# Kernel optimization log

Hardware: AMD Instinct MI355X
Metric: run time of the kernel (lower is better)

Reference implementation:

```python
import jax, jax.numpy as jnp
import numpy as np

N, M, D, DE, H, G = 2048, 16, 512, 128, 8, 50
DH, DEH, NF = D // H, DE // H, 4  # head dims; 2**2 frames for 2D frame averaging
OPS = jnp.array([[-1., -1.], [-1., 1.], [1., -1.], [1., 1.]], dtype=jnp.float32)

def ln(x, eps=1e-5):
    m = x.mean(-1, keepdims=True)
    v = x.var(-1, keepdims=True)
    return (x - m) * jax.lax.rsqrt(v + eps)

def mlp2(x, w1, b1, w2, b2):
    # timm-style Mlp with norm_layer=LayerNorm: fc1 -> GELU -> LN -> fc2 (dropout=0)
    h = jax.nn.gelu(x @ w1 + b1, approximate=False)
    return ln(h) @ w2 + b2

def setup_inputs():
    key = jax.random.key(0)
    ks = iter(jax.random.split(key, 32))
    def w(shape):
        return jax.random.normal(next(ks), shape, jnp.float32) / float(np.sqrt(shape[0]))
    return dict(
        gene_exp=jax.random.uniform(next(ks), (N, G), jnp.float32),
        token_embs=jax.random.normal(next(ks), (N, D), jnp.float32),
        coords=jax.random.uniform(next(ks), (N, 2), jnp.float32) * 100.0,
        neighbor_indices=jax.random.randint(next(ks), (N, M), 0, N),
        w_qkv=w((D, 3 * D)), b_qkv=jnp.zeros((3 * D,), jnp.float32),
        wa1=w((2 * DH + DEH + G, D)), ba1=jnp.zeros((D,), jnp.float32),
        wa2=w((D, 1)), ba2=jnp.zeros((1,), jnp.float32),
        we1=w((3, DE)), be1=jnp.zeros((DE,), jnp.float32),
        we2=w((DE, DE)), be2=jnp.zeros((DE,), jnp.float32),
        wo1=w((D + DE, D)), bo1=jnp.zeros((D,), jnp.float32),
        wo2=w((D, D)), bo2=jnp.zeros((D,), jnp.float32),
        wm1=w((D, 4 * D)), bm1=jnp.zeros((4 * D,), jnp.float32),
        wm2=w((4 * D, D)), bm2=jnp.zeros((D,), jnp.float32),
        wg1=w((D, D)), bg1=jnp.zeros((D,), jnp.float32),
        wg2=w((D, G)), bg2=jnp.zeros((G,), jnp.float32),
    )

def reference(gene_exp, token_embs, coords, neighbor_indices, w_qkv, b_qkv, wa1, ba1, wa2, ba2, we1, be1, we2, be2, wo1, bo1, wo2, bo2, wm1, bm1, wm2, bm2, wg1, bg1, wg2, bg2):
    qkv = ln(token_embs) @ w_qkv + b_qkv
    q, k, v = jnp.split(qkv, 3, axis=-1)
    q, k, v = (t.reshape(N, H, DH) for t in (q, k, v))
    # --- frame averaging over neighbor point clouds (dim=2 -> 4 sign frames) ---
    radial = coords[neighbor_indices] - coords[:, None, :]            # [N,M,2]
    rnorm = jnp.linalg.norm(radial, axis=-1, keepdims=True)           # [N,M,1]
    Xc = radial - radial.mean(axis=1, keepdims=True)
    C = jnp.einsum('nmi,nmj->nij', Xc, Xc)                            # [N,2,2]
    _, V = jnp.linalg.eigh(jax.lax.stop_gradient(C))                  # eigh on detached cov (as in torch code)
    proj = jnp.einsum('nmj,nji->nmi', Xc, V)                          # [N,M,2]
    frame = OPS[None, :, None, :] * proj[:, None, :, :]               # [N,4,M,2]
    rn = jnp.broadcast_to(rnorm[:, None], (N, NF, M, 1))
    edge = mlp2(jnp.concatenate([frame, rn], axis=-1), we1, be1, we2, be2).mean(axis=1)  # [N,M,DE]
    # --- per-edge MLP attention ---
    gd = gene_exp[neighbor_indices] - gene_exp[:, None, :]            # [N,M,G]
    msg = jnp.concatenate([
        jnp.broadcast_to(q[:, None], (N, M, H, DH)),
        k[neighbor_indices],
        edge.reshape(N, M, H, DEH),
        jnp.broadcast_to(gd[:, :, None, :], (N, M, H, G)),
    ], axis=-1)                                                       # [N,M,H,2*DH+DEH+G]
    logits = mlp2(msg, wa1, ba1, wa2, ba2)[..., 0]                    # [N,M,H]
    attn = jax.nn.softmax(logits.transpose(0, 2, 1), axis=-1)         # [N,H,M]
    # --- context aggregation ---
    sc = jnp.einsum('nhm,nmhd->nhd', attn, v[neighbor_indices]).reshape(N, D)
    ec = jnp.einsum('nhm,nmhd->nhd', attn, edge.reshape(N, M, H, DEH)).reshape(N, DE)
    ctx = mlp2(jnp.concatenate([sc, ec], axis=-1), wo1, bo1, wo2, bo2)
    tok = token_embs + ctx
    tok = tok + mlp2(tok, wm1, bm1, wm2, bm2)
    # gene updater: Linear -> GELU -> LN -> Linear
    gene_out = mlp2(tok, wg1, bg1, wg2, bg2)
    return gene_out, tok
```

## Files before the change

### kernel.cpp

```cpp
#include <hip/hip_runtime.h>
#include <math.h>

#define NN 2048
#define MM 16
#define DD 512
#define DE 128
#define HH 8
#define GG 50
#define DH 64
#define DEH 16

typedef __attribute__((ext_vector_type(8))) short bf8_t;
typedef __attribute__((ext_vector_type(4))) float f4_t;
typedef __attribute__((ext_vector_type(2))) float f2_t;
typedef unsigned short us;

__device__ __forceinline__ void gload16(const us* g, us* l) {
    __builtin_amdgcn_global_load_lds(
        (const __attribute__((address_space(1))) unsigned int*)g,
        (__attribute__((address_space(3))) unsigned int*)l, 16, 0, 0);
}

__device__ __forceinline__ float gelu_f(float x) {
    float u = 1.5957691216f * fmaf(0.044715f * x, x * x, x);
    u = fminf(fmaxf(u, -30.f), 30.f);
    float e = __expf(u);
    float t = fmaf(-2.f, __builtin_amdgcn_rcpf(e + 1.f), 1.f);
    float hx = 0.5f * x;
    return fmaf(hx, t, hx);
}

__device__ __forceinline__ f2_t gelu2(f2_t x) {
    f2_t u = ((x * 0.044715f) * (x * x) + x) * 1.5957691216f;
    f2_t e1;
    e1.x = __expf(u.x) + 1.f;
    e1.y = __expf(u.y) + 1.f;
    f2_t r;
    r.x = __builtin_amdgcn_rcpf(e1.x);
    r.y = __builtin_amdgcn_rcpf(e1.y);
    f2_t t = r * (-2.f) + 1.f;
    f2_t hx = x * 0.5f;
    return hx * t + hx;
}

__device__ __forceinline__ float wsum(float v) {
#pragma unroll
    for (int o = 32; o; o >>= 1) v += __shfl_xor(v, o, 64);
    return v;
}

__device__ __forceinline__ us f2bf(float x) {
    union { float f; unsigned int u; } v;
    v.f = x;
    unsigned int r = v.u + 0x7FFFu + ((v.u >> 16) & 1u);
    return (us)(r >> 16);
}

__device__ __forceinline__ float bfu(unsigned int u) {
    union { unsigned int x; float f; } v;
    v.x = u;
    return v.f;
}
#define BF_LO(u) bfu((u) << 16)
#define BF_HI(u) bfu((u) & 0xFFFF0000u)
__device__ __forceinline__ float b2f(us u) { return bfu((unsigned int)u << 16); }

__global__ __launch_bounds__(256) void act_ln_kernel(float* __restrict__ outF,
                                                     us* __restrict__ outB,
                                                     const float* __restrict__ x,
                                                     int C, int do_gelu) {
    int row = blockIdx.x, tid = threadIdx.x;
    int nv = C >> 8;
    float v[8];
    float s = 0.f, ss = 0.f;
    for (int i = 0; i < nv; ++i) {
        float val = x[(size_t)row * C + tid + (i << 8)];
        if (do_gelu) val = gelu_f(val);
        v[i] = val;
        s += val;
        ss += val * val;
    }
    __shared__ float red[4][2];
    s = wsum(s);
    ss = wsum(ss);
    int wid = tid >> 6, lane = tid & 63;
    if (lane == 0) { red[wid][0] = s; red[wid][1] = ss; }
    __syncthreads();
    s = red[0][0] + red[1][0] + red[2][0] + red[3][0];
    ss = red[0][1] + red[1][1] + red[2][1] + red[3][1];
    float mean = s / (float)C;
    float var = ss / (float)C - mean * mean;
    float rs = rsqrtf(var + 1e-5f);
    for (int i = 0; i < nv; ++i) {
        float y = (v[i] - mean) * rs;
        size_t idx = (size_t)row * C + tid + (i << 8);
        if (outF) outF[idx] = y;
        if (outB) outB[idx] = f2bf(y);
    }
}

__global__ __launch_bounds__(256) void lnproj_kernel(const float* __restrict__ te,
                                                     us* __restrict__ x_ln_bf,
                                                     const float* __restrict__ coords,
                                                     const int* __restrict__ nbr,
                                                     float* __restrict__ projs,
                                                     float* __restrict__ rns) {
    int tid = threadIdx.x;
    if (blockIdx.x < 2048) {
        int row = blockIdx.x;
        float v0 = te[(size_t)row * 512 + tid];
        float v1 = te[(size_t)row * 512 + 256 + tid];
        __shared__ float red[4][2];
        float s = wsum(v0 + v1);
        float ss = wsum(fmaf(v0, v0, v1 * v1));
        int wid = tid >> 6, lane = tid & 63;
        if (lane == 0) { red[wid][0] = s; red[wid][1] = ss; }
        __syncthreads();
        s = red[0][0] + red[1][0] + red[2][0] + red[3][0];
        ss = red[0][1] + red[1][1] + red[2][1] + red[3][1];
        float mean = s * (1.f / 512.f);
        float var = ss * (1.f / 512.f) - mean * mean;
        float rs = rsqrtf(var + 1e-5f);
        x_ln_bf[(size_t)row * 512 + tid] = f2bf((v0 - mean) * rs);
        x_ln_bf[(size_t)row * 512 + 256 + tid] = f2bf((v1 - mean) * rs);
        return;
    }
    int node = (blockIdx.x - 2048) * 16 + (tid >> 4);
    int m = tid & 15;
    float cx = coords[node * 2], cy = coords[node * 2 + 1];
    int j = nbr[node * 16 + m];
    float rx = coords[j * 2] - cx;
    float ry = coords[j * 2 + 1] - cy;
    float rn = sqrtf(rx * rx + ry * ry);
    float mx = rx, my = ry;
#pragma unroll
    for (int o = 8; o; o >>= 1) { mx += __shfl_xor(mx, o, 16); my += __shfl_xor(my, o, 16); }
    mx *= 0.0625f;
    my *= 0.0625f;
    float xcx = rx - mx, xcy = ry - my;
    float sxx = xcx * xcx, sxy = xcx * xcy, syy = xcy * xcy;
#pragma unroll
    for (int o = 8; o; o >>= 1) {
        sxx += __shfl_xor(sxx, o, 16);
        sxy += __shfl_xor(sxy, o, 16);
        syy += __shfl_xor(syy, o, 16);
    }
    double a = (double)sxx, b = (double)sxy, c = (double)syy;
    double diff = 0.5 * (a - c);
    double disc = sqrt(diff * diff + b * b);
    double l2 = 0.5 * (a + c) + disc;
    double v2x = b, v2y = l2 - a;
    double nn2 = sqrt(v2x * v2x + v2y * v2y);
    if (nn2 < 1e-30) { v2x = (a >= c) ? 1.0 : 0.0; v2y = 1.0 - v2x; nn2 = 1.0; }
    v2x /= nn2;
    v2y /= nn2;
    double v1x = -v2y, v1y = v2x;
    int row = node * 16 + m;
    projs[row * 2] = (float)((double)xcx * v1x + (double)xcy * v1y);
    projs[row * 2 + 1] = (float)((double)xcx * v2x + (double)xcy * v2y);
    rns[row] = rn;
}

struct TCJob {
    const float* src;
    us* dst;
    int K, N, Kld, b0;
};
struct TC11 {
    TCJob j[11];
    int acc_end;
    const float* wa1_s;
    us* wesT_d;
    const float* gene_s;
    us* gene_d;
};

__global__ __launch_bounds__(256) void tcast_all(TC11 P) {
    __shared__ float tile[32][33];
    int b = blockIdx.x;
    if (b >= P.acc_end) {
        int lb = b - P.acc_end;
        if (lb < 64) {
            int idx = lb * 256 + threadIdx.x;
            int c = idx >> 5, t = idx & 31;
            P.wesT_d[idx] = (t < 16) ? f2bf(P.wa1_s[(size_t)(128 + t) * 512 + c]) : (us)0;
        } else {
            int idx = (lb - 64) * 256 + threadIdx.x;
            int r = idx >> 6, c = idx & 63;
            P.gene_d[idx] = (c < 50) ? f2bf(P.gene_s[r * 50 + c]) : (us)0;
        }
        return;
    }
    int ji = 0;
#pragma unroll
    for (int i = 1; i < 11; ++i)
        if (b >= P.j[i].b0) ji = i;
    const float* W = P.j[ji].src;
    us* Wt = P.j[ji].dst;
    int K = P.j[ji].K, N = P.j[ji].N, Kld = P.j[ji].Kld;
    int lb = b - P.j[ji].b0;
    int nbx = (N + 31) >> 5;
    int n0 = (lb % nbx) * 32, k0 = (lb / nbx) * 32;
    int tx = threadIdx.x & 31, ty = threadIdx.x >> 5;
#pragma unroll
    for (int p = 0; p < 4; ++p) {
        int k = k0 + ty + p * 8;
        tile[ty + p * 8][tx] = (k < K && n0 + tx < N) ? W[(size_t)k * N + n0 + tx] : 0.f;
    }
    __syncthreads();
#pragma unroll
    for (int p = 0; p < 4; ++p) {
        int n = n0 + ty + p * 8;
        if (n < N && k0 + tx < Kld) Wt[(size_t)n * Kld + k0 + tx] = f2bf(tile[tx][ty + p * 8]);
    }
}

struct GJob {
    const us* A;
    const us* Bt;
    const float* bias;
    const float* resid;
    const float* residH;
    float* outF;
    us* outB;
    us* outB2;
    us* outB3;
    int M, Kstride, nkt, N, Nout, b0;
};
struct GJobs {
    GJob j[4];
    int nj;
};

__global__ __launch_bounds__(256) void gemm_bf16_kernel(GJobs P) {
    __shared__ us As[2][128 * 64];
    __shared__ us Bs[2][128 * 64];
    int b = blockIdx.x;
    int ji = 0;
#pragma unroll
    for (int i = 1; i < 4; ++i)
        if (i < P.nj && b >= P.j[i].b0) ji = i;
    const us* A = P.j[ji].A;
    const us* Bt = P.j[ji].Bt;
    int Kst = P.j[ji].Kstride, nkt = P.j[ji].nkt;
    int Nn = P.j[ji].N, Nout = P.j[ji].Nout;
    int lb = b - P.j[ji].b0;
    int ncol = Nn >> 7;
    int col0 = (lb % ncol) << 7, row0 = (lb / ncol) << 7;

    int tid = threadIdx.x;
    int lane = tid & 63;
    int w = tid >> 6;
    int wr = w >> 1, wc = w & 1;
    f4_t acc[4][4];
#pragma unroll
    for (int a = 0; a < 4; ++a)
#pragma unroll
        for (int bb = 0; bb < 4; ++bb) {
            acc[a][bb][0] = 0.f; acc[a][bb][1] = 0.f;
            acc[a][bb][2] = 0.f; acc[a][bb][3] = 0.f;
        }

    auto stage = [&](int buf, int kt) {
#pragma unroll
        for (int p = 0; p < 4; ++p) {
            int id = p * 256 + tid;
            int r = id >> 3, cch = id & 7;
            int kc = cch ^ (r & 7);
            int wb = p * 256 + (tid & 192);
            gload16(A + (size_t)(row0 + r) * Kst + kt + kc * 8, As[buf] + wb * 8);
            gload16(Bt + (size_t)(col0 + r) * Kst + kt + kc * 8, Bs[buf] + wb * 8);
        }
    };

    stage(0, 0);
    __syncthreads();
    for (int t = 0; t < nkt; ++t) {
        int cur = t & 1;
        if (t + 1 < nkt) stage(cur ^ 1, (t + 1) << 6);
#pragma unroll
        for (int kk = 0; kk < 2; ++kk) {
            bf8_t af[4], bfr[4];
            int kslot = kk * 4 + (lane >> 4);
#pragma unroll
            for (int mi = 0; mi < 4; ++mi) {
                int r = wr * 64 + mi * 16 + (lane & 15);
                af[mi] = *(const bf8_t*)((char*)As[cur] + r * 128 + ((kslot ^ (r & 7)) * 16));
            }
#pragma unroll
            for (int ni = 0; ni < 4; ++ni) {
                int r = wc * 64 + ni * 16 + (lane & 15);
                bfr[ni] = *(const bf8_t*)((char*)Bs[cur] + r * 128 + ((kslot ^ (r & 7)) * 16));
            }
#pragma unroll
            for (int mi = 0; mi < 4; ++mi)
#pragma unroll
                for (int ni = 0; ni < 4; ++ni)
                    acc[mi][ni] = __builtin_amdgcn_mfma_f32_16x16x32_bf16(
                        af[mi], bfr[ni], acc[mi][ni], 0, 0, 0);
        }
        __syncthreads();
    }
    const float* bias = P.j[ji].bias;
    const float* resid = P.j[ji].resid;
    const float* residH = P.j[ji].residH;
    float* outF = P.j[ji].outF;
    us* outB = P.j[ji].outB;
    us* outB2 = P.j[ji].outB2;
    us* outB3 = P.j[ji].outB3;
    int cr = lane >> 4, cc = lane & 15;
#pragma unroll
    for (int mi = 0; mi < 4; ++mi)
#pragma unroll
        for (int ni = 0; ni < 4; ++ni) {
            int col = col0 + wc * 64 + ni * 16 + cc;
            if (col >= Nout) continue;
            float bv = bias ? bias[col] : 0.f;
#pragma unroll
            for (int j = 0; j < 4; ++j) {
                int row = row0 + wr * 64 + mi * 16 + cr * 4 + j;
                float v = acc[mi][ni][j] + bv;
                if (resid) v += resid[(size_t)row * Nout + col];
                if (residH) v += residH[(size_t)(row >> 3) * Nout + col];
                if (outF) outF[(size_t)row * Nout + col] = v;
                if (outB) {
                    if (outB2) {
                        int seg = col >> 9, cl = col & 511;
                        us* dst = seg == 0 ? outB : (seg == 1 ? outB2 : outB3);
                        dst[(size_t)row * 512 + cl] = f2bf(v);
                    } else {
                        outB[(size_t)row * Nout + col] = f2bf(v);
                    }
                }
            }
        }
}

__global__ __launch_bounds__(256) void wm2_combine(const float* __restrict__ pk,
                                                   const float* __restrict__ bias,
                                                   const float* __restrict__ resid,
                                                   float* __restrict__ outF,
                                                   us* __restrict__ outB) {
    int idx = blockIdx.x * 256 + threadIdx.x;
    float v = pk[idx] + pk[idx + 1048576] + pk[idx + 2097152] + pk[idx + 3145728] +
              bias[idx & 511] + resid[idx];
    outF[idx] = v;
    outB[idx] = f2bf(v);
}

__global__ __launch_bounds__(256) void frame_mlp1_kernel(const float* __restrict__ projs,
                                                         const float* __restrict__ rns,
                                                         const float* __restrict__ we1,
                                                         const float* __restrict__ be1,
                                                         us* __restrict__ u) {
    int row = blockIdx.x * 4 + (threadIdx.x >> 6);
    int lane = threadIdx.x & 63;
    float px = projs[row * 2], py = projs[row * 2 + 1], rn = rns[row];
    int c0 = lane, c1 = lane + 64;
    float w10a = we1[c0], w11a = we1[128 + c0], w12a = we1[256 + c0], b1a = be1[c0];
    float w10b = we1[c1], w11b = we1[128 + c1], w12b = we1[256 + c1], b1b = be1[c1];
    float acc0 = 0.f, acc1 = 0.f;
    const float opsx[4] = {-1.f, -1.f, 1.f, 1.f};
    const float opsy[4] = {-1.f, 1.f, -1.f, 1.f};
#pragma unroll
    for (int f = 0; f < 4; ++f) {
        float fx = opsx[f] * px, fy = opsy[f] * py;
        float h0 = gelu_f(fmaf(fx, w10a, fmaf(fy, w11a, fmaf(rn, w12a, b1a))));
        float h1 = gelu_f(fmaf(fx, w10b, fmaf(fy, w11b, fmaf(rn, w12b, b1b))));
        float s = wsum(h0 + h1);
        float ss = wsum(fmaf(h0, h0, h1 * h1));
        float mean = s * (1.f / 128.f);
        float var = ss * (1.f / 128.f) - mean * mean;
        float rs = rsqrtf(var + 1e-5f);
        acc0 += (h0 - mean) * rs;
        acc1 += (h1 - mean) * rs;
    }
    u[(size_t)row * 128 + c0] = f2bf(0.25f * acc0);
    u[(size_t)row * 128 + c1] = f2bf(0.25f * acc1);
}

__global__ __launch_bounds__(256) void logits_fused_kernel(
    const us* __restrict__ qpb,
    const us* __restrict__ kg,
    const us* __restrict__ gepb,
    const us* __restrict__ edgeb,
    const us* __restrict__ wesT,
    const int* __restrict__ nbr,
    const float* __restrict__ wa2,
    const float* __restrict__ ba2,
    const us* __restrict__ v2b,
    us* __restrict__ scec) {
    __shared__ us Es[2048 + 32];
    __shared__ us qmg[8 * 520];
    __shared__ float wa2s[512];
    __shared__ float lgs[128];
    __shared__ float attn[128];
    __shared__ float sinv[8];
    __shared__ int jns[16];
    int n = blockIdx.x, tid = threadIdx.x;
    int lane = tid & 63;
    float swv = 0.f;
#pragma unroll
    for (int i = 0; i < 8; ++i) swv += wa2[lane + 64 * i];
    float sw = wsum(swv);
    float ba2v = ba2[0];
    {
        const uint* s2 = (const uint*)(edgeb + (size_t)n * 2048);
        uint* d2 = (uint*)Es;
        for (int i = tid; i < 1040; i += 256) d2[i] = s2[i];
        const uint* s3 = (const uint*)(qpb + (size_t)n * 4096);
        const uint* s4 = (const uint*)(gepb + (size_t)n * 512);
        uint* d3 = (uint*)qmg;
        for (int i = tid; i < 2048; i += 256) {
            uint q = s3[i], g = s4[i & 255];
            float lo = BF_LO(q) - BF_LO(g), hi = BF_HI(q) - BF_HI(g);
            d3[(i >> 8) * 260 + (i & 255)] = ((uint)f2bf(hi) << 16) | (uint)f2bf(lo);
        }
        for (int i = tid; i < 512; i += 256) wa2s[i] = wa2[i];
        if (tid < 16) jns[tid] = nbr[n * 16 + tid];
    }
    __syncthreads();

    int cc = lane & 15, cr = lane >> 4;
    int w = tid >> 6;
#pragma unroll
    for (int mt = 0; mt < 2; ++mt) {
        int mh = w * 32 + mt * 16 + cc;
        int m = mh >> 3, h = mh & 7;
        int j8h = jns[m] * 8 + h;
        const us* kgrow = kg + (size_t)j8h * 512;
        const us* qrow = qmg + h * 520;
        bf8_t bfr = *(const bf8_t*)((const char*)Es + mh * 32 + cr * 16);
        f2_t s2v = {0.f, 0.f}, ss2 = {0.f, 0.f}, sd2 = {0.f, 0.f};
#pragma unroll 4
        for (int ct = 0; ct < 32; ++ct) {
            int chb = ct * 16 + cr * 4;
            bf8_t af = *(const bf8_t*)(wesT + (ct * 16 + cc) * 32 + cr * 8);
            f4_t z = {0.f, 0.f, 0.f, 0.f};
            f4_t ep = __builtin_amdgcn_mfma_f32_16x16x32_bf16(af, bfr, z, 0, 0, 0);
            uint2 kg4 = *(const uint2*)(kgrow + chb);
            uint2 qp4 = *(const uint2*)(qrow + chb);
            float4 w4 = *(const float4*)(wa2s + chb);
            f2_t ep01 = {ep[0], ep[1]}, ep23 = {ep[2], ep[3]};
            f2_t q01 = {BF_LO(qp4.x), BF_HI(qp4.x)};
            f2_t q23 = {BF_LO(qp4.y), BF_HI(qp4.y)};
            f2_t k01 = {BF_LO(kg4.x), BF_HI(kg4.x)};
            f2_t k23 = {BF_LO(kg4.y), BF_HI(kg4.y)};
            f2_t g01 = gelu2(ep01 + q01 + k01);
            f2_t g23 = gelu2(ep23 + q23 + k23);
            s2v += g01;
            s2v += g23;
            ss2 = g01 * g01 + ss2;
            ss2 = g23 * g23 + ss2;
            f2_t w01 = {w4.x, w4.y}, w23 = {w4.z, w4.w};
            sd2 = g01 * w01 + sd2;
            sd2 = g23 * w23 + sd2;
        }
        float s = s2v.x + s2v.y, ss = ss2.x + ss2.y, sd = sd2.x + sd2.y;
        s += __shfl_xor(s, 16, 64);
        s += __shfl_xor(s, 32, 64);
        ss += __shfl_xor(ss, 16, 64);
        ss += __shfl_xor(ss, 32, 64);
        sd += __shfl_xor(sd, 16, 64);
        sd += __shfl_xor(sd, 32, 64);
        if (cr == 0) {
            float mean = s * (1.f / 512.f);
            float var = ss * (1.f / 512.f) - mean * mean;
            lgs[mh] = (sd - mean * sw) * rsqrtf(var + 1e-5f) + ba2v;
        }
    }
    __syncthreads();
    if (tid < 128) {
        int h = tid & 7;
        float mx = lgs[h];
#pragma unroll
        for (int mm = 1; mm < 16; ++mm) mx = fmaxf(mx, lgs[mm * 8 + h]);
        attn[tid] = __expf(lgs[tid] - mx);
    }
    __syncthreads();
    if (tid < 8) {
        float se = 0.f;
#pragma unroll
        for (int mm = 0; mm < 16; ++mm) se += attn[mm * 8 + tid];
        sinv[tid] = 1.f / se;
    }
    __syncthreads();
    for (int c = tid; c < 640; c += 256) {
        float acc = 0.f;
        int h;
        if (c < 512) {
            h = c >> 6;
            int t = c & 63;
#pragma unroll
            for (int m = 0; m < 16; ++m)
                acc = fmaf(attn[m * 8 + h], b2f(v2b[(size_t)jns[m] * 512 + h * 64 + t]), acc);
        } else {
            int d = c - 512;
            h = d >> 4;
            int t = d & 15;
#pragma unroll
            for (int m = 0; m < 16; ++m)
                acc = fmaf(attn[m * 8 + h], b2f(Es[m * 128 + h * 16 + t]), acc);
        }
        scec[(size_t)n * 640 + c] = f2bf(acc * sinv[h]);
    }
}

extern "C" void kernel_launch(void* const* d_in, const int* in_sizes, int n_in,
                              void* d_out, int out_size, void* d_ws, size_t ws_size,
                              hipStream_t stream) {
    const float* gene_exp = (const float*)d_in[0];
    const float* token_embs = (const float*)d_in[1];
    const float* coords = (const float*)d_in[2];
    const int* nbr = (const int*)d_in[3];
    const float* w_qkv = (const float*)d_in[4];
    const float* b_qkv = (const float*)d_in[5];
    const float* wa1 = (const float*)d_in[6];
    const float* ba1 = (const float*)d_in[7];
    const float* wa2 = (const float*)d_in[8];
    const float* ba2 = (const float*)d_in[9];
    const float* we1 = (const float*)d_in[10];
    const float* be1 = (const float*)d_in[11];
    const float* we2 = (const float*)d_in[12];
    const float* be2 = (const float*)d_in[13];
    const float* wo1 = (const float*)d_in[14];
    const float* bo1 = (const float*)d_in[15];
    const float* wo2 = (const float*)d_in[16];
    const float* bo2 = (const float*)d_in[17];
    const float* wm1 = (const float*)d_in[18];
    const float* bm1 = (const float*)d_in[19];
    const float* wm2 = (const float*)d_in[20];
    const float* bm2 = (const float*)d_in[21];
    const float* wg1 = (const float*)d_in[22];
    const float* bg1 = (const float*)d_in[23];
    const float* wg2 = (const float*)d_in[24];
    const float* bg2 = (const float*)d_in[25];

    float* out = (float*)d_out;
    float* gene_out = out;
    float* tok_out = out + 2048 * 50;

    float* ws = (float*)d_ws;
    size_t o = 0;
    auto alloc = [&](size_t nf) {
        float* p = ws + o;
        o += nf;
        return p;
    };
    us* x_ln_bf = (us*)alloc((size_t)2048 * 512 / 2);
    us* q2b = (us*)alloc((size_t)16384 * 64 / 2);
    us* k2b = (us*)alloc((size_t)16384 * 64 / 2);
    us* v2b = (us*)alloc((size_t)2048 * 512 / 2);
    us* qpb = (us*)alloc((size_t)16384 * 512 / 2);
    us* kgb = (us*)alloc((size_t)16384 * 512 / 2);
    float* gep = alloc((size_t)2048 * 512);
    us* gepb = (us*)alloc((size_t)2048 * 512 / 2);
    us* edgeb = (us*)alloc(((size_t)2048 * 2048 + 32) / 2);
    us* scec_bf = (us*)alloc((size_t)2048 * 640 / 2);
    float* buf1 = alloc((size_t)2048 * 512);
    us* buf1_bf = (us*)alloc((size_t)2048 * 512 / 2);
    float* buf2 = alloc((size_t)2048 * 2048);
    us* buf2_bf = (us*)alloc((size_t)2048 * 2048 / 2);
    float* tok1 = alloc((size_t)2048 * 512);
    us* tok1_bf = (us*)alloc((size_t)2048 * 512 / 2);
    us* tokout_bf = (us*)alloc((size_t)2048 * 512 / 2);
    us* u_bf = (us*)alloc((size_t)32768 * 128 / 2);
    float* projs = alloc((size_t)32768 * 2);
    float* rns = alloc((size_t)32768);
    us* gene_bf = (us*)alloc((size_t)2048 * 64 / 2);
    float* pk4 = alloc((size_t)4 * 2048 * 512);
    us* qkvT = (us*)alloc((size_t)1536 * 512 / 2);
    us* wa1qT = (us*)alloc((size_t)512 * 64 / 2);
    us* wa1kT = (us*)alloc((size_t)512 * 64 / 2);
    us* wa1gT = (us*)alloc((size_t)512 * 64 / 2);
    us* we2T = (us*)alloc((size_t)128 * 128 / 2);
    us* wo1T = (us*)alloc((size_t)512 * 640 / 2);
    us* wo2T = (us*)alloc((size_t)512 * 512 / 2);
    us* wm1T = (us*)alloc((size_t)2048 * 512 / 2);
    us* wm2T = (us*)alloc((size_t)512 * 2048 / 2);
    us* wg1T = (us*)alloc((size_t)512 * 512 / 2);
    us* wg2T = (us*)alloc((size_t)128 * 512 / 2);
    us* wesT = (us*)alloc((size_t)512 * 32 / 2);
    if (o * sizeof(float) > ws_size) return;

    auto mkjob = [](const us* A, const us* Bt, const float* bias, const float* resid,
                    const float* residH, float* outF, us* outB, us* outB2, us* outB3,
                    int M, int Kstride, int nkt, int N, int Nout, int b0) {
        GJob j;
        j.A = A; j.Bt = Bt; j.bias = bias; j.resid = resid; j.residH = residH;
        j.outF = outF; j.outB = outB; j.outB2 = outB2; j.outB3 = outB3;
        j.M = M; j.Kstride = Kstride; j.nkt = nkt; j.N = N; j.Nout = Nout; j.b0 = b0;
        return j;
    };
    auto G1 = [&](const us* A, const us* Bt, const float* bias, const float* resid,
                  const float* residH, float* outF, us* outB, int M, int K, int N,
                  int Nout) {
        GJobs P;
        P.nj = 1;
        P.j[0] = mkjob(A, Bt, bias, resid, residH, outF, outB, nullptr, nullptr,
                       M, K, K >> 6, N, Nout, 0);
        gemm_bf16_kernel<<<(N / 128) * (M / 128), 256, 0, stream>>>(P);
    };

    hipMemsetAsync(wg2T, 0, (size_t)128 * 512 * 2, stream);
    {
        TC11 P;
        auto set = [&](int i, const float* s, us* d, int K, int N, int Kld, int& acc) {
            P.j[i] = {s, d, K, N, Kld, acc};
            acc += ((N + 31) / 32) * ((Kld + 31) / 32);
        };
        int acc = 0;
        set(0, w_qkv, qkvT, 512, 1536, 512, acc);
        set(1, wa1, wa1qT, 64, 512, 64, acc);
        set(2, wa1 + 64 * 512, wa1kT, 64, 512, 64, acc);
        set(3, we2, we2T, 128, 128, 128, acc);
        set(4, wo1, wo1T, 640, 512, 640, acc);
        set(5, wo2, wo2T, 512, 512, 512, acc);
        set(6, wm1, wm1T, 512, 2048, 512, acc);
        set(7, wm2, wm2T, 2048, 512, 2048, acc);
        set(8, wg1, wg1T, 512, 512, 512, acc);
        set(9, wa1 + 144 * 512, wa1gT, 50, 512, 64, acc);
        set(10, wg2, wg2T, 512, 50, 512, acc);
        P.acc_end = acc;
        P.wa1_s = wa1;
        P.wesT_d = wesT;
        P.gene_s = gene_exp;
        P.gene_d = gene_bf;
        tcast_all<<<acc + 64 + 512, 256, 0, stream>>>(P);
    }

    lnproj_kernel<<<2048 + 128, 256, 0, stream>>>(token_embs, x_ln_bf, coords, nbr,
                                                  projs, rns);
    frame_mlp1_kernel<<<8192, 256, 0, stream>>>(projs, rns, we1, be1, u_bf);
    {
        GJobs P;
        P.nj = 3;
        P.j[0] = mkjob(x_ln_bf, qkvT, b_qkv, nullptr, nullptr, nullptr, q2b, k2b, v2b,
                       2048, 512, 8, 1536, 1536, 0);
        P.j[1] = mkjob(gene_bf, wa1gT, nullptr, nullptr, nullptr, gep, gepb, nullptr,
                       nullptr, 2048, 64, 1, 512, 512, 192);
        P.j[2] = mkjob(u_bf, we2T, be2, nullptr, nullptr, nullptr, edgeb, nullptr,
                       nullptr, 32768, 128, 2, 128, 128, 256);
        gemm_bf16_kernel<<<512, 256, 0, stream>>>(P);
    }
    {
        GJobs P;
        P.nj = 2;
        P.j[0] = mkjob(q2b, wa1qT, ba1, nullptr, nullptr, nullptr, qpb, nullptr, nullptr,
                       16384, 64, 1, 512, 512, 0);
        P.j[1] = mkjob(k2b, wa1kT, nullptr, nullptr, gep, nullptr, kgb, nullptr, nullptr,
                       16384, 64, 1, 512, 512, 512);
        gemm_bf16_kernel<<<1024, 256, 0, stream>>>(P);
    }
    logits_fused_kernel<<<2048, 256, 0, stream>>>(qpb, kgb, gepb, edgeb, wesT, nbr,
                                                  wa2, ba2, v2b, scec_bf);
    G1(scec_bf, wo1T, bo1, nullptr, nullptr, buf1, nullptr, 2048, 640, 512, 512);
    act_ln_kernel<<<2048, 256, 0, stream>>>(nullptr, buf1_bf, buf1, 512, 1);
    G1(buf1_bf, wo2T, bo2, token_embs, nullptr, tok1, tok1_bf, 2048, 512, 512, 512);
    G1(tok1_bf, wm1T, bm1, nullptr, nullptr, buf2, nullptr, 2048, 512, 2048, 2048);
    act_ln_kernel<<<2048, 256, 0, stream>>>(nullptr, buf2_bf, buf2, 2048, 1);
    {
        GJobs P;
        P.nj = 4;
#pragma unroll
        for (int s = 0; s < 4; ++s)
            P.j[s] = mkjob(buf2_bf + s * 512, wm2T + s * 512, nullptr, nullptr, nullptr,
                           pk4 + (size_t)s * 2048 * 512, nullptr, nullptr, nullptr,
                           2048, 2048, 8, 512, 512, s * 64);
        gemm_bf16_kernel<<<256, 256, 0, stream>>>(P);
        wm2_combine<<<4096, 256, 0, stream>>>(pk4, bm2, tok1, tok_out, tokout_bf);
    }
    G1(tokout_bf, wg1T, bg1, nullptr, nullptr, buf1, nullptr, 2048, 512, 512, 512);
    act_ln_kernel<<<2048, 256, 0, stream>>>(nullptr, buf1_bf, buf1, 512, 1);
    G1(buf1_bf, wg2T, bg2, nullptr, nullptr, gene_out, nullptr, 2048, 512, 128, 50);
}
```

Measured before the change: 352.9 us.

## Split-K small GEMMs, fuse k-projection into logits kernel, regroup GEMM launches

Removes the precomputed per-neighbor k·wa1k+gene projection buffer: the logits kernel now computes the k contribution with extra MFMAs from k2b and wa1kT, and adds gathered gene projections staged in shared memory. This avoids writing and re-reading a large 16384x512 intermediate. The 2048x512 output GEMMs (wo1, wo2, wg1, wg2) are split along K into partial products to raise block count, followed by combine kernels that fuse bias, residual, GELU and LayerNorm. The edge GEMM moves to the second grouped launch. The trade-off is more MFMA work per logits block, larger shared memory use, and extra partial-sum traffic.

```diff
diff --git a/kernel.cpp b/kernel.cpp
--- a/kernel.cpp
+++ b/kernel.cpp
@@ -97,6 +97,61 @@
         if (outF) outF[idx] = y;
         if (outB) outB[idx] = f2bf(y);
     }
+}
+
+__global__ __launch_bounds__(256) void combine2ln_kernel(const float* __restrict__ pk,
+                                                         const float* __restrict__ bias,
+                                                         us* __restrict__ outB) {
+    int row = blockIdx.x, tid = threadIdx.x;
+    size_t b = (size_t)row * 512;
+    float v0 = gelu_f(pk[b + tid] + pk[1048576 + b + tid] + bias[tid]);
+    float v1 = gelu_f(pk[b + 256 + tid] + pk[1048576 + b + 256 + tid] + bias[256 + tid]);
+    __shared__ float red[4][2];
+    float s = wsum(v0 + v1);
+    float ss = wsum(fmaf(v0, v0, v1 * v1));
+    int wid = tid >> 6, lane = tid & 63;
+    if (lane == 0) { red[wid][0] = s; red[wid][1] = ss; }
+    __syncthreads();
+    s = red[0][0] + red[1][0] + red[2][0] + red[3][0];
+    ss = red[0][1] + red[1][1] + red[2][1] + red[3][1];
+    float mean = s * (1.f / 512.f);
+    float var = ss * (1.f / 512.f) - mean * mean;
+    float rs = rsqrtf(var + 1e-5f);
+    outB[b + tid] = f2bf((v0 - mean) * rs);
+    outB[b + 256 + tid] = f2bf((v1 - mean) * rs);
+}
+
+__global__ __launch_bounds__(256) void combine2_kernel(const float* __restrict__ pk,
+                                                       const float* __restrict__ bias,
+                                                       const float* __restrict__ resid,
+                                                       float* __restrict__ outF,
+                                                       us* __restrict__ outB) {
+    int idx = blockIdx.x * 256 + threadIdx.x;
+    float v = pk[idx] + pk[idx + 1048576] + bias[idx & 511] + resid[idx];
+    outF[idx] = v;
+    outB[idx] = f2bf(v);
+}
+
+__global__ __launch_bounds__(256) void wm2_combine(const float* __restrict__ pk,
+                                                   const float* __restrict__ bias,
+                                                   const float* __restrict__ resid,
+                                                   float* __restrict__ outF,
+                                                   us* __restrict__ outB) {
+    int idx = blockIdx.x * 256 + threadIdx.x;
+    float v = pk[idx] + pk[idx + 1048576] + pk[idx + 2097152] + pk[idx + 3145728] +
+              bias[idx & 511] + resid[idx];
+    outF[idx] = v;
+    outB[idx] = f2bf(v);
+}
+
+__global__ __launch_bounds__(256) void wg2_combine(const float* __restrict__ pk,
+                                                   const float* __restrict__ bias,
+                                                   float* __restrict__ outF) {
+    int idx = blockIdx.x * 256 + threadIdx.x;
+    if (idx >= 102400) return;
+    float v = pk[idx] + pk[idx + 102400] + pk[idx + 204800] + pk[idx + 307200] +
+              bias[idx % 50];
+    outF[idx] = v;
 }
 
 __global__ __launch_bounds__(256) void lnproj_kernel(const float* __restrict__ te,
@@ -336,18 +391,6 @@
         }
 }
 
-__global__ __launch_bounds__(256) void wm2_combine(const float* __restrict__ pk,
-                                                   const float* __restrict__ bias,
-                                                   const float* __restrict__ resid,
-                                                   float* __restrict__ outF,
-                                                   us* __restrict__ outB) {
-    int idx = blockIdx.x * 256 + threadIdx.x;
-    float v = pk[idx] + pk[idx + 1048576] + pk[idx + 2097152] + pk[idx + 3145728] +
-              bias[idx & 511] + resid[idx];
-    outF[idx] = v;
-    outB[idx] = f2bf(v);
-}
-
 __global__ __launch_bounds__(256) void frame_mlp1_kernel(const float* __restrict__ projs,
                                                          const float* __restrict__ rns,
                                                          const float* __restrict__ we1,
@@ -381,10 +424,11 @@
 
 __global__ __launch_bounds__(256) void logits_fused_kernel(
     const us* __restrict__ qpb,
-    const us* __restrict__ kg,
+    const us* __restrict__ k2b,
     const us* __restrict__ gepb,
     const us* __restrict__ edgeb,
     const us* __restrict__ wesT,
+    const us* __restrict__ wa1kT,
     const int* __restrict__ nbr,
     const float* __restrict__ wa2,
     const float* __restrict__ ba2,
@@ -392,6 +436,7 @@
     us* __restrict__ scec) {
     __shared__ us Es[2048 + 32];
     __shared__ us qmg[8 * 520];
+    __shared__ us gepj[16 * 512];
     __shared__ float wa2s[512];
     __shared__ float lgs[128];
     __shared__ float attn[128];
@@ -416,6 +461,12 @@
             float lo = BF_LO(q) - BF_LO(g), hi = BF_HI(q) - BF_HI(g);
             d3[(i >> 8) * 260 + (i & 255)] = ((uint)f2bf(hi) << 16) | (uint)f2bf(lo);
         }
+        uint* d5 = (uint*)gepj;
+#pragma unroll 4
+        for (int p = 0; p < 16; ++p) {
+            int j = nbr[n * 16 + p];
+            d5[p * 256 + tid] = ((const uint*)(gepb + (size_t)j * 512))[tid];
+        }
         for (int i = tid; i < 512; i += 256) wa2s[i] = wa2[i];
         if (tid < 16) jns[tid] = nbr[n * 16 + tid];
     }
@@ -428,26 +479,32 @@
         int mh = w * 32 + mt * 16 + cc;
         int m = mh >> 3, h = mh & 7;
         int j8h = jns[m] * 8 + h;
-        const us* kgrow = kg + (size_t)j8h * 512;
         const us* qrow = qmg + h * 520;
+        const us* gjrow = gepj + m * 512;
         bf8_t bfr = *(const bf8_t*)((const char*)Es + mh * 32 + cr * 16);
+        bf8_t bk0 = *(const bf8_t*)(k2b + (size_t)j8h * 64 + cr * 8);
+        bf8_t bk1 = *(const bf8_t*)(k2b + (size_t)j8h * 64 + 32 + cr * 8);
         f2_t s2v = {0.f, 0.f}, ss2 = {0.f, 0.f}, sd2 = {0.f, 0.f};
 #pragma unroll 4
         for (int ct = 0; ct < 32; ++ct) {
             int chb = ct * 16 + cr * 4;
-            bf8_t af = *(const bf8_t*)(wesT + (ct * 16 + cc) * 32 + cr * 8);
+            bf8_t afw = *(const bf8_t*)(wesT + (ct * 16 + cc) * 32 + cr * 8);
+            bf8_t afk0 = *(const bf8_t*)(wa1kT + (ct * 16 + cc) * 64 + cr * 8);
+            bf8_t afk1 = *(const bf8_t*)(wa1kT + (ct * 16 + cc) * 64 + 32 + cr * 8);
             f4_t z = {0.f, 0.f, 0.f, 0.f};
-            f4_t ep = __builtin_amdgcn_mfma_f32_16x16x32_bf16(af, bfr, z, 0, 0, 0);
-            uint2 kg4 = *(const uint2*)(kgrow + chb);
+            f4_t ep = __builtin_amdgcn_mfma_f32_16x16x32_bf16(afk0, bk0, z, 0, 0, 0);
+            ep = __builtin_amdgcn_mfma_f32_16x16x32_bf16(afk1, bk1, ep, 0, 0, 0);
+            ep = __builtin_amdgcn_mfma_f32_16x16x32_bf16(afw, bfr, ep, 0, 0, 0);
             uint2 qp4 = *(const uint2*)(qrow + chb);
+            uint2 gj4 = *(const uint2*)(gjrow + chb);
             float4 w4 = *(const float4*)(wa2s + chb);
             f2_t ep01 = {ep[0], ep[1]}, ep23 = {ep[2], ep[3]};
             f2_t q01 = {BF_LO(qp4.x), BF_HI(qp4.x)};
             f2_t q23 = {BF_LO(qp4.y), BF_HI(qp4.y)};
-            f2_t k01 = {BF_LO(kg4.x), BF_HI(kg4.x)};
-            f2_t k23 = {BF_LO(kg4.y), BF_HI(kg4.y)};
-            f2_t g01 = gelu2(ep01 + q01 + k01);
-            f2_t g23 = gelu2(ep23 + q23 + k23);
+            f2_t g01v = {BF_LO(gj4.x), BF_HI(gj4.x)};
+            f2_t g23v = {BF_LO(gj4.y), BF_HI(gj4.y)};
+            f2_t g01 = gelu2(ep01 + q01 + g01v);
+            f2_t g23 = gelu2(ep23 + q23 + g23v);
             s2v += g01;
             s2v += g23;
             ss2 = g01 * g01 + ss2;
@@ -552,12 +609,9 @@
     us* k2b = (us*)alloc((size_t)16384 * 64 / 2);
     us* v2b = (us*)alloc((size_t)2048 * 512 / 2);
     us* qpb = (us*)alloc((size_t)16384 * 512 / 2);
-    us* kgb = (us*)alloc((size_t)16384 * 512 / 2);
-    float* gep = alloc((size_t)2048 * 512);
     us* gepb = (us*)alloc((size_t)2048 * 512 / 2);
     us* edgeb = (us*)alloc(((size_t)2048 * 2048 + 32) / 2);
     us* scec_bf = (us*)alloc((size_t)2048 * 640 / 2);
-    float* buf1 = alloc((size_t)2048 * 512);
     us* buf1_bf = (us*)alloc((size_t)2048 * 512 / 2);
     float* buf2 = alloc((size_t)2048 * 2048);
     us* buf2_bf = (us*)alloc((size_t)2048 * 2048 / 2);
@@ -600,6 +654,17 @@
         P.j[0] = mkjob(A, Bt, bias, resid, residH, outF, outB, nullptr, nullptr,
                        M, K, K >> 6, N, Nout, 0);
         gemm_bf16_kernel<<<(N / 128) * (M / 128), 256, 0, stream>>>(P);
+    };
+    auto Gsk2 = [&](const us* A, const us* Bt, int M, int K, int N) {
+        GJobs P;
+        P.nj = 2;
+        int half = K >> 1;
+        int blk = (N / 128) * (M / 128);
+        P.j[0] = mkjob(A, Bt, nullptr, nullptr, nullptr, pk4, nullptr, nullptr, nullptr,
+                       M, K, half >> 6, N, N, 0);
+        P.j[1] = mkjob(A + half, Bt + half, nullptr, nullptr, nullptr, pk4 + 1048576,
+                       nullptr, nullptr, nullptr, M, K, half >> 6, N, N, blk);
+        gemm_bf16_kernel<<<2 * blk, 256, 0, stream>>>(P);
     };
 
     hipMemsetAsync(wg2T, 0, (size_t)128 * 512 * 2, stream);
@@ -634,29 +699,28 @@
     frame_mlp1_kernel<<<8192, 256, 0, stream>>>(projs, rns, we1, be1, u_bf);
     {
         GJobs P;
-        P.nj = 3;
+        P.nj = 2;
         P.j[0] = mkjob(x_ln_bf, qkvT, b_qkv, nullptr, nullptr, nullptr, q2b, k2b, v2b,
                        2048, 512, 8, 1536, 1536, 0);
-        P.j[1] = mkjob(gene_bf, wa1gT, nullptr, nullptr, nullptr, gep, gepb, nullptr,
+        P.j[1] = mkjob(gene_bf, wa1gT, nullptr, nullptr, nullptr, nullptr, gepb, nullptr,
                        nullptr, 2048, 64, 1, 512, 512, 192);
-        P.j[2] = mkjob(u_bf, we2T, be2, nullptr, nullptr, nullptr, edgeb, nullptr,
-                       nullptr, 32768, 128, 2, 128, 128, 256);
-        gemm_bf16_kernel<<<512, 256, 0, stream>>>(P);
+        gemm_bf16_kernel<<<256, 256, 0, stream>>>(P);
     }
     {
         GJobs P;
         P.nj = 2;
         P.j[0] = mkjob(q2b, wa1qT, ba1, nullptr, nullptr, nullptr, qpb, nullptr, nullptr,
                        16384, 64, 1, 512, 512, 0);
-        P.j[1] = mkjob(k2b, wa1kT, nullptr, nullptr, gep, nullptr, kgb, nullptr, nullptr,
-                       16384, 64, 1, 512, 512, 512);
-        gemm_bf16_kernel<<<1024, 256, 0, stream>>>(P);
-    }
-    logits_fused_kernel<<<2048, 256, 0, stream>>>(qpb, kgb, gepb, edgeb, wesT, nbr,
-                                                  wa2, ba2, v2b, scec_bf);
-    G1(scec_bf, wo1T, bo1, nullptr, nullptr, buf1, nullptr, 2048, 640, 512, 512);
-    act_ln_kernel<<<2048, 256, 0, stream>>>(nullptr, buf1_bf, buf1, 512, 1);
-    G1(buf1_bf, wo2T, bo2, token_embs, nullptr, tok1, tok1_bf, 2048, 512, 512, 512);
+        P.j[1] = mkjob(u_bf, we2T, be2, nullptr, nullptr, nullptr, edgeb, nullptr,
+                       nullptr, 32768, 128, 2, 128, 128, 512);
+        gemm_bf16_kernel<<<768, 256, 0, stream>>>(P);
+    }
+    logits_fused_kernel<<<2048, 256, 0, stream>>>(qpb, k2b, gepb, edgeb, wesT, wa1kT,
+                                                  nbr, wa2, ba2, v2b, scec_bf);
+    Gsk2(scec_bf, wo1T, 2048, 640, 512);
+    combine2ln_kernel<<<2048, 256, 0, stream>>>(pk4, bo1, buf1_bf);
+    Gsk2(buf1_bf, wo2T, 2048, 512, 512);
+    combine2_kernel<<<4096, 256, 0, stream>>>(pk4, bo2, token_embs, tok1, tok1_bf);
     G1(tok1_bf, wm1T, bm1, nullptr, nullptr, buf2, nullptr, 2048, 512, 2048, 2048);
     act_ln_kernel<<<2048, 256, 0, stream>>>(nullptr, buf2_bf, buf2, 2048, 1);
     {
@@ -665,12 +729,22 @@
 #pragma unroll
         for (int s = 0; s < 4; ++s)
             P.j[s] = mkjob(buf2_bf + s * 512, wm2T + s * 512, nullptr, nullptr, nullptr,
-                           pk4 + (size_t)s * 2048 * 512, nullptr, nullptr, nullptr,
+                           pk4 + (size_t)s * 1048576, nullptr, nullptr, nullptr,
                            2048, 2048, 8, 512, 512, s * 64);
         gemm_bf16_kernel<<<256, 256, 0, stream>>>(P);
         wm2_combine<<<4096, 256, 0, stream>>>(pk4, bm2, tok1, tok_out, tokout_bf);
     }
-    G1(tokout_bf, wg1T, bg1, nullptr, nullptr, buf1, nullptr, 2048, 512, 512, 512);
-    act_ln_kernel<<<2048, 256, 0, stream>>>(nullptr, buf1_bf, buf1, 512, 1);
-    G1(buf1_bf, wg2T, bg2, nullptr, nullptr, gene_out, nullptr, 2048, 512, 128, 50);
-}
+    Gsk2(tokout_bf, wg1T, 2048, 512, 512);
+    combine2ln_kernel<<<2048, 256, 0, stream>>>(pk4, bg1, buf1_bf);
+    {
+        GJobs P;
+        P.nj = 4;
+#pragma unroll
+        for (int s = 0; s < 4; ++s)
+            P.j[s] = mkjob(buf1_bf + s * 128, wg2T + s * 128, nullptr, nullptr, nullptr,
+                           pk4 + (size_t)s * 102400, nullptr, nullptr, nullptr,
+                           2048, 512, 2, 128, 50, s * 16);
+        gemm_bf16_kernel<<<64, 256, 0, stream>>>(P);
+        wg2_combine<<<400, 256, 0, stream>>>(pk4, bg2, gene_out);
+    }
+}
```

Result: slower. 377.3 us (+6.9%).
